# Kernel tuning notes

Measured on AMD Instinct MI355X. Metric: run time of the kernel, lower is better.

Reference implementation:

```python
import jax, jax.numpy as jnp
import numpy as np

N_HEAD = 16
D_HEAD = 64
D_MODEL = 1024
LN_EPS = 1e-5


def layer_norm(x, gamma, beta):
    mu = jnp.mean(x, axis=-1, keepdims=True)
    var = jnp.mean((x - mu) ** 2, axis=-1, keepdims=True)
    return (x - mu) * jax.lax.rsqrt(var + LN_EPS) * gamma + beta


def setup_inputs() -> dict:
    key = jax.random.key(0)
    ks = jax.random.split(key, 6)
    B, T = 2, 2048
    inp = jax.random.normal(ks[0], (B, T, D_MODEL), dtype=jnp.float32)
    # qkv_net: Linear(d_model, 3*n_head*d_head)
    W_qkv = jax.random.normal(ks[1], (3 * N_HEAD * D_HEAD, D_MODEL), dtype=jnp.float32) * (D_MODEL ** -0.5)
    b_qkv = jax.random.normal(ks[2], (3 * N_HEAD * D_HEAD,), dtype=jnp.float32) * 0.02
    # o_net: Linear(n_head*d_head, d_model, bias=False)
    W_o = jax.random.normal(ks[3], (D_MODEL, N_HEAD * D_HEAD), dtype=jnp.float32) * ((N_HEAD * D_HEAD) ** -0.5)
    gamma = jnp.ones((D_MODEL,), dtype=jnp.float32)
    beta = jnp.zeros((D_MODEL,), dtype=jnp.float32)
    return {"inp": inp, "W_qkv": W_qkv, "b_qkv": b_qkv, "W_o": W_o, "gamma": gamma, "beta": beta}


def reference(inp, W_qkv, b_qkv, W_o, gamma, beta):
    B, T, D = inp.shape
    H, dh = N_HEAD, D_HEAD
    scale = 1.0 / (dh ** 0.5)

    qkv = inp @ W_qkv.T + b_qkv                      # (B, T, 3*H*dh)
    head_q, head_k, head_v = jnp.split(qkv, 3, axis=2)
    # (B, T, H, dh) -> (B, H, T, dh)
    q = head_q.reshape(B, T, H, dh).transpose(0, 2, 1, 3)
    k = head_k.reshape(B, T, H, dh).transpose(0, 2, 1, 3)
    v = head_v.reshape(B, T, H, dh).transpose(0, 2, 1, 3)

    attn_score = jnp.einsum('bhqd,bhkd->bhqk', q, k) * scale  # (B, H, T, T)
    attn_prob = jax.nn.softmax(attn_score, axis=-1)           # dropatt is identity in eval
    attn_vec = jnp.einsum('bhqk,bhkd->bhqd', attn_prob, v)    # (B, H, T, dh)

    # Faithful to original: (B*H, T, dh) batch-major buffer is VIEWED as (H, B, T, dh)
    attn_vec = attn_vec.reshape(H, B, T, dh)
    attn_vec = attn_vec.transpose(1, 2, 0, 3).reshape(B, T, H * dh)

    attn_out = attn_vec @ W_o.T                                # dropout identity in eval
    return layer_norm(inp + attn_out, gamma, beta)
```

## Files before the change

### kernel.cpp

```cpp
#include <hip/hip_runtime.h>
#include <hip/hip_bf16.h>
#include <stdint.h>

typedef __bf16 bf16_t;
typedef __bf16 bf16x8 __attribute__((ext_vector_type(8)));
typedef __bf16 bf16x4 __attribute__((ext_vector_type(4)));
typedef float floatx4 __attribute__((ext_vector_type(4)));

#define QSCALE 0.180336879f

__device__ static inline void gll16(const void* g, void* l) {
    __builtin_amdgcn_global_load_lds((const __attribute__((address_space(1))) void*)g,
                                     (__attribute__((address_space(3))) void*)l, 16, 0, 0);
}

__global__ __launch_bounds__(256) void cvt_f32_bf16(const float* __restrict__ in,
                                                    bf16_t* __restrict__ out, int n4) {
    int i = blockIdx.x * 256 + threadIdx.x;
    if (i < n4) {
        float4 v = ((const float4*)in)[i];
        bf16x4 o;
        o[0] = (bf16_t)v.x; o[1] = (bf16_t)v.y; o[2] = (bf16_t)v.z; o[3] = (bf16_t)v.w;
        ((bf16x4*)out)[i] = o;
    }
}

__global__ __launch_bounds__(256, 3)
void gemm_qkv(const bf16_t* __restrict__ A, const bf16_t* __restrict__ Bw,
              const float* __restrict__ bias,
              bf16_t* __restrict__ qk, bf16_t* __restrict__ vT) {
    constexpr int K = 1024;
    __shared__ bf16_t lA[128 * 32];
    __shared__ bf16_t lB[128 * 32];
    const int tid  = threadIdx.x;
    const int lane = tid & 63, wave = tid >> 6;
    const int quad = lane >> 4, l16 = lane & 15;
    const int wy = wave >> 1, wx = wave & 1;
    const int bm = blockIdx.y * 128, bn = blockIdx.x * 128;

    const int c0 = tid, c1 = tid + 256;
    const bf16_t* Ap0 = A + (size_t)(bm + (c0 >> 2)) * K + (c0 & 3) * 8;
    const bf16_t* Ap1 = A + (size_t)(bm + (c1 >> 2)) * K + (c1 & 3) * 8;
    const bf16_t* Bp0 = Bw + (size_t)(bn + (c0 >> 2)) * K + (c0 & 3) * 8;
    const bf16_t* Bp1 = Bw + (size_t)(bn + (c1 >> 2)) * K + (c1 & 3) * 8;
    bf16_t* dA0 = &lA[(wave * 64) * 8];
    bf16_t* dA1 = &lA[(256 + wave * 64) * 8];
    bf16_t* dB0 = &lB[(wave * 64) * 8];
    bf16_t* dB1 = &lB[(256 + wave * 64) * 8];

    floatx4 acc[4][4] = {};

    for (int kt = 0; kt < K; kt += 32) {
        __syncthreads();
        gll16(Ap0 + kt, dA0);
        gll16(Ap1 + kt, dA1);
        gll16(Bp0 + kt, dB0);
        gll16(Bp1 + kt, dB1);
        __syncthreads();
        bf16x8 af[4], bfr[4];
#pragma unroll
        for (int i = 0; i < 4; i++) {
            af[i]  = *(const bf16x8*)(lA + (wy * 64 + i * 16 + l16) * 32 + quad * 8);
            bfr[i] = *(const bf16x8*)(lB + (wx * 64 + i * 16 + l16) * 32 + quad * 8);
        }
#pragma unroll
        for (int i = 0; i < 4; i++)
#pragma unroll
            for (int j = 0; j < 4; j++)
                acc[i][j] = __builtin_amdgcn_mfma_f32_16x16x32_bf16(af[i], bfr[j], acc[i][j], 0, 0, 0);
    }

    const bool is_v = (bn >= 2048);
#pragma unroll
    for (int j = 0; j < 4; j++) {
        const int n = bn + wx * 64 + j * 16 + l16;
        const float bv = bias[n];
        const bool isq = (n < 1024);
#pragma unroll
        for (int i = 0; i < 4; i++) {
            const int mbase = bm + wy * 64 + i * 16 + quad * 4;
            if (!is_v) {
#pragma unroll
                for (int r = 0; r < 4; r++) {
                    float c = acc[i][j][r] + bv;
                    if (isq) c *= QSCALE;
                    qk[(size_t)(mbase + r) * 2048 + n] = (bf16_t)c;
                }
            } else {
                const int nn = n - 2048;
                const int b  = mbase >> 11;
                const int t  = mbase & 2047;
                const int vrow = b * 1024 + nn;
                bf16x4 pack;
#pragma unroll
                for (int r = 0; r < 4; r++) pack[r] = (bf16_t)(acc[i][j][r] + bv);
                *(bf16x4*)(vT + (size_t)vrow * 2048 + t) = pack;
            }
        }
    }
}

__global__ __launch_bounds__(256, 2)
void attn_kernel(const bf16_t* __restrict__ qk, const bf16_t* __restrict__ vT,
                 bf16_t* __restrict__ av) {
    __shared__ bf16_t Kbuf[2][64 * 72];
    __shared__ bf16_t Vbuf[2][64 * 72];
    __shared__ bf16_t Pbuf[4][2][16 * 72];
    const int tid  = threadIdx.x;
    const int lane = tid & 63, wave = tid >> 6;
    const int quad = lane >> 4, l16 = lane & 15;
    const int bid = blockIdx.x;
    const int s  = bid & 31;
    const int hl = (s & 7) * 4 + (s >> 3);
    const int qt = bid >> 5;
    const int b = hl >> 4, h = hl & 15;

    const bf16_t* Qbase = qk + (size_t)(b * 2048 + qt * 128 + wave * 32) * 2048 + h * 64;
    const bf16_t* Kbase = qk + (size_t)(b * 2048) * 2048 + 1024 + h * 64;
    const bf16_t* Vbase = vT + (size_t)(hl * 64) * 2048;

    const int sr = tid >> 3;
    const int sc = (tid & 7) * 8;
    const bf16_t* Kg = Kbase + (size_t)sr * 2048 + sc;
    const bf16_t* Vg = Vbase + (size_t)sr * 2048 + sc;

    bf16x8 qf[2][2];
#pragma unroll
    for (int rt = 0; rt < 2; rt++)
#pragma unroll
        for (int kc = 0; kc < 2; kc++)
            qf[rt][kc] = *(const bf16x8*)(Qbase + (size_t)(rt * 16 + l16) * 2048 + kc * 32 + quad * 8);

    floatx4 accO[2][4] = {};
    float lacc[2] = {0.f, 0.f};

    {
        bf16x8 k0 = *(const bf16x8*)(Kg);
        bf16x8 k1 = *(const bf16x8*)(Kg + (size_t)32 * 2048);
        bf16x8 v0 = *(const bf16x8*)(Vg);
        bf16x8 v1 = *(const bf16x8*)(Vg + (size_t)32 * 2048);
        *(bf16x8*)&Kbuf[0][sr * 72 + sc] = k0;
        *(bf16x8*)&Kbuf[0][(sr + 32) * 72 + sc] = k1;
        *(bf16x8*)&Vbuf[0][sr * 72 + sc] = v0;
        *(bf16x8*)&Vbuf[0][(sr + 32) * 72 + sc] = v1;
    }

    for (int it = 0; it < 32; ++it) {
        const int cur = it & 1;
        __syncthreads();
        bf16x8 gk0, gk1, gv0, gv1;
        if (it < 31) {
            const bf16_t* kg = Kg + (size_t)(it + 1) * 64 * 2048;
            const bf16_t* vg = Vg + (it + 1) * 64;
            gk0 = *(const bf16x8*)(kg);
            gk1 = *(const bf16x8*)(kg + (size_t)32 * 2048);
            gv0 = *(const bf16x8*)(vg);
            gv1 = *(const bf16x8*)(vg + (size_t)32 * 2048);
        }
        floatx4 st[2][4] = {};
#pragma unroll
        for (int nt = 0; nt < 4; nt++) {
            const bf16_t* kr = &Kbuf[cur][(nt * 16 + l16) * 72 + quad * 8];
            bf16x8 k0 = *(const bf16x8*)(kr);
            bf16x8 k1 = *(const bf16x8*)(kr + 32);
            st[0][nt] = __builtin_amdgcn_mfma_f32_16x16x32_bf16(k0, qf[0][0], st[0][nt], 0, 0, 0);
            st[0][nt] = __builtin_amdgcn_mfma_f32_16x16x32_bf16(k1, qf[0][1], st[0][nt], 0, 0, 0);
            st[1][nt] = __builtin_amdgcn_mfma_f32_16x16x32_bf16(k0, qf[1][0], st[1][nt], 0, 0, 0);
            st[1][nt] = __builtin_amdgcn_mfma_f32_16x16x32_bf16(k1, qf[1][1], st[1][nt], 0, 0, 0);
        }
#pragma unroll
        for (int rt = 0; rt < 2; rt++) {
            float ls = 0.f;
#pragma unroll
            for (int nt = 0; nt < 4; nt++) {
                bf16x4 pk;
#pragma unroll
                for (int r = 0; r < 4; r++) {
                    float p = exp2f(st[rt][nt][r]);
                    ls += p;
                    pk[r] = (bf16_t)p;
                }
                *(bf16x4*)&Pbuf[wave][rt][l16 * 72 + nt * 16 + quad * 4] = pk;
            }
            lacc[rt] += ls;
        }
#pragma unroll
        for (int kc2 = 0; kc2 < 2; kc2++) {
            bf16x8 pf0 = *(const bf16x8*)&Pbuf[wave][0][l16 * 72 + kc2 * 32 + quad * 8];
            bf16x8 pf1 = *(const bf16x8*)&Pbuf[wave][1][l16 * 72 + kc2 * 32 + quad * 8];
#pragma unroll
            for (int ct = 0; ct < 4; ct++) {
                bf16x8 vf = *(const bf16x8*)&Vbuf[cur][(ct * 16 + l16) * 72 + kc2 * 32 + quad * 8];
                accO[0][ct] = __builtin_amdgcn_mfma_f32_16x16x32_bf16(pf0, vf, accO[0][ct], 0, 0, 0);
                accO[1][ct] = __builtin_amdgcn_mfma_f32_16x16x32_bf16(pf1, vf, accO[1][ct], 0, 0, 0);
            }
        }
        if (it < 31) {
            const int nxt = cur ^ 1;
            *(bf16x8*)&Kbuf[nxt][sr * 72 + sc] = gk0;
            *(bf16x8*)&Kbuf[nxt][(sr + 32) * 72 + sc] = gk1;
            *(bf16x8*)&Vbuf[nxt][sr * 72 + sc] = gv0;
            *(bf16x8*)&Vbuf[nxt][(sr + 32) * 72 + sc] = gv1;
        }
    }

    float linv[2];
#pragma unroll
    for (int rt = 0; rt < 2; rt++) {
        float l = lacc[rt];
        l += __shfl_xor(l, 16);
        l += __shfl_xor(l, 32);
        linv[rt] = 1.0f / l;
    }
    const int b2 = hl & 1;
    const int colb = (hl >> 1) * 64;
    bf16_t* outb = av + (size_t)(b2 * 2048 + qt * 128 + wave * 32) * 1024 + colb;
#pragma unroll
    for (int rt = 0; rt < 2; rt++) {
        float invq[4];
#pragma unroll
        for (int r = 0; r < 4; r++) invq[r] = __shfl(linv[rt], quad * 4 + r);
#pragma unroll
        for (int ct = 0; ct < 4; ct++)
#pragma unroll
            for (int r = 0; r < 4; r++)
                outb[(size_t)(rt * 16 + quad * 4 + r) * 1024 + ct * 16 + l16] =
                    (bf16_t)(accO[rt][ct][r] * invq[r]);
    }
}

__global__ __launch_bounds__(256, 3)
void gemm_o(const bf16_t* __restrict__ A, const bf16_t* __restrict__ Bw,
            float* __restrict__ out) {
    constexpr int K = 1024;
    __shared__ bf16_t lA[128 * 32];
    __shared__ bf16_t lB[128 * 32];
    const int tid  = threadIdx.x;
    const int lane = tid & 63, wave = tid >> 6;
    const int quad = lane >> 4, l16 = lane & 15;
    const int wy = wave >> 1, wx = wave & 1;
    const int bm = blockIdx.y * 128, bn = blockIdx.x * 128;

    const int c0 = tid, c1 = tid + 256;
    const bf16_t* Ap0 = A + (size_t)(bm + (c0 >> 2)) * K + (c0 & 3) * 8;
    const bf16_t* Ap1 = A + (size_t)(bm + (c1 >> 2)) * K + (c1 & 3) * 8;
    const bf16_t* Bp0 = Bw + (size_t)(bn + (c0 >> 2)) * K + (c0 & 3) * 8;
    const bf16_t* Bp1 = Bw + (size_t)(bn + (c1 >> 2)) * K + (c1 & 3) * 8;
    bf16_t* dA0 = &lA[(wave * 64) * 8];
    bf16_t* dA1 = &lA[(256 + wave * 64) * 8];
    bf16_t* dB0 = &lB[(wave * 64) * 8];
    bf16_t* dB1 = &lB[(256 + wave * 64) * 8];

    floatx4 acc[4][4] = {};
    for (int kt = 0; kt < K; kt += 32) {
        __syncthreads();
        gll16(Ap0 + kt, dA0);
        gll16(Ap1 + kt, dA1);
        gll16(Bp0 + kt, dB0);
        gll16(Bp1 + kt, dB1);
        __syncthreads();
        bf16x8 af[4], bfr[4];
#pragma unroll
        for (int i = 0; i < 4; i++) {
            af[i]  = *(const bf16x8*)(lA + (wy * 64 + i * 16 + l16) * 32 + quad * 8);
            bfr[i] = *(const bf16x8*)(lB + (wx * 64 + i * 16 + l16) * 32 + quad * 8);
        }
#pragma unroll
        for (int i = 0; i < 4; i++)
#pragma unroll
            for (int j = 0; j < 4; j++)
                acc[i][j] = __builtin_amdgcn_mfma_f32_16x16x32_bf16(af[i], bfr[j], acc[i][j], 0, 0, 0);
    }
#pragma unroll
    for (int j = 0; j < 4; j++) {
        const int n = bn + wx * 64 + j * 16 + l16;
#pragma unroll
        for (int i = 0; i < 4; i++) {
            const int mbase = bm + wy * 64 + i * 16 + quad * 4;
#pragma unroll
            for (int r = 0; r < 4; r++)
                out[(size_t)(mbase + r) * 1024 + n] = acc[i][j][r];
        }
    }
}

__global__ __launch_bounds__(256)
void ln_kernel(const float* __restrict__ inp, const float* __restrict__ ao,
               const float* __restrict__ gamma, const float* __restrict__ beta,
               float* __restrict__ out) {
    const int row = blockIdx.x, tid = threadIdx.x;
    const int wave = tid >> 6, lane = tid & 63;
    float4 a = ((const float4*)(inp + (size_t)row * 1024))[tid];
    float4 c = ((const float4*)(ao + (size_t)row * 1024))[tid];
    float x0 = a.x + c.x, x1 = a.y + c.y, x2 = a.z + c.z, x3 = a.w + c.w;
    float s = x0 + x1 + x2 + x3;
    float sq = x0 * x0 + x1 * x1 + x2 * x2 + x3 * x3;
#pragma unroll
    for (int mm = 32; mm >= 1; mm >>= 1) {
        s += __shfl_xor(s, mm);
        sq += __shfl_xor(sq, mm);
    }
    __shared__ float rs[4], rq[4];
    if (lane == 0) { rs[wave] = s; rq[wave] = sq; }
    __syncthreads();
    s = rs[0] + rs[1] + rs[2] + rs[3];
    sq = rq[0] + rq[1] + rq[2] + rq[3];
    const float mu = s * (1.0f / 1024.0f);
    const float var = sq * (1.0f / 1024.0f) - mu * mu;
    const float rstd = rsqrtf(var + 1e-5f);
    float4 g = ((const float4*)gamma)[tid], bt = ((const float4*)beta)[tid];
    float4 o;
    o.x = (x0 - mu) * rstd * g.x + bt.x;
    o.y = (x1 - mu) * rstd * g.y + bt.y;
    o.z = (x2 - mu) * rstd * g.z + bt.z;
    o.w = (x3 - mu) * rstd * g.w + bt.w;
    ((float4*)(out + (size_t)row * 1024))[tid] = o;
}

extern "C" void kernel_launch(void* const* d_in, const int* in_sizes, int n_in,
                              void* d_out, int out_size, void* d_ws, size_t ws_size,
                              hipStream_t stream) {
    const float* inp   = (const float*)d_in[0];
    const float* Wqkv  = (const float*)d_in[1];
    const float* bqkv  = (const float*)d_in[2];
    const float* Wo    = (const float*)d_in[3];
    const float* gamma = (const float*)d_in[4];
    const float* beta  = (const float*)d_in[5];
    float* out = (float*)d_out;

    char* ws = (char*)d_ws;
    bf16_t* inp_bf  = (bf16_t*)(ws);
    bf16_t* wqkv_bf = (bf16_t*)(ws + (8u << 20));
    bf16_t* wo_bf   = (bf16_t*)(ws + (14u << 20));
    bf16_t* qk_buf  = (bf16_t*)(ws + (16u << 20));
    bf16_t* vT_buf  = (bf16_t*)(ws + (32u << 20));
    bf16_t* av_buf  = (bf16_t*)(ws + (40u << 20));
    float*  ao_buf  = (float*)(ws + (48u << 20));

    cvt_f32_bf16<<<4096, 256, 0, stream>>>(inp, inp_bf, 4096 * 1024 / 4);
    cvt_f32_bf16<<<3072, 256, 0, stream>>>(Wqkv, wqkv_bf, 3072 * 1024 / 4);
    cvt_f32_bf16<<<1024, 256, 0, stream>>>(Wo, wo_bf, 1024 * 1024 / 4);

    gemm_qkv<<<dim3(24, 32), 256, 0, stream>>>(inp_bf, wqkv_bf, bqkv, qk_buf, vT_buf);
    attn_kernel<<<512, 256, 0, stream>>>(qk_buf, vT_buf, av_buf);
    gemm_o<<<dim3(8, 32), 256, 0, stream>>>(av_buf, wo_bf, ao_buf);
    ln_kernel<<<4096, 256, 0, stream>>>(inp, ao_buf, gamma, beta, out);
}
```

Baseline: 222.4 us.

## Fuse conversions, split attention LDS layout, shrink gemm_o tiles, raise occupancy

Three f32-to-bf16 conversion launches are merged into one kernel that picks its source by block index, saving launch overhead. The attention kernel moves from padded 72-wide LDS rows to two unpadded 32-wide halves, raises launch bounds to 3 blocks per CU, and uses the hardware exp2 builtin. It also processes the P·V product one row tile at a time. gemm_o switches to 64x128 tiles with twice as many blocks and 4 blocks per CU to fill the machine better. The attention change leaves a dead loop and computes exp2 twice per score, and the unpadded LDS rows may cause bank conflicts.

Result: faster. 210.4 us (-5.4%).

```diff
diff --git a/kernel.cpp b/kernel.cpp
--- a/kernel.cpp
+++ b/kernel.cpp
@@ -14,15 +14,23 @@
                                      (__attribute__((address_space(3))) void*)l, 16, 0, 0);
 }
 
-__global__ __launch_bounds__(256) void cvt_f32_bf16(const float* __restrict__ in,
-                                                    bf16_t* __restrict__ out, int n4) {
-    int i = blockIdx.x * 256 + threadIdx.x;
-    if (i < n4) {
-        float4 v = ((const float4*)in)[i];
-        bf16x4 o;
-        o[0] = (bf16_t)v.x; o[1] = (bf16_t)v.y; o[2] = (bf16_t)v.z; o[3] = (bf16_t)v.w;
-        ((bf16x4*)out)[i] = o;
-    }
+__global__ __launch_bounds__(256) void cvt_all(const float* __restrict__ inp,
+                                               const float* __restrict__ wqkv,
+                                               const float* __restrict__ wo,
+                                               bf16_t* __restrict__ o_inp,
+                                               bf16_t* __restrict__ o_wqkv,
+                                               bf16_t* __restrict__ o_wo) {
+    int blk = blockIdx.x;
+    const float* src;
+    bf16_t* dst;
+    if (blk < 4096)      { src = inp;  dst = o_inp; }
+    else if (blk < 7168) { src = wqkv; dst = o_wqkv; blk -= 4096; }
+    else                 { src = wo;   dst = o_wo;   blk -= 7168; }
+    int i = blk * 256 + threadIdx.x;
+    float4 v = ((const float4*)src)[i];
+    bf16x4 o;
+    o[0] = (bf16_t)v.x; o[1] = (bf16_t)v.y; o[2] = (bf16_t)v.z; o[3] = (bf16_t)v.w;
+    ((bf16x4*)dst)[i] = o;
 }
 
 __global__ __launch_bounds__(256, 3)
@@ -100,12 +108,12 @@
     }
 }
 
-__global__ __launch_bounds__(256, 2)
+__global__ __launch_bounds__(256, 3)
 void attn_kernel(const bf16_t* __restrict__ qk, const bf16_t* __restrict__ vT,
                  bf16_t* __restrict__ av) {
-    __shared__ bf16_t Kbuf[2][64 * 72];
-    __shared__ bf16_t Vbuf[2][64 * 72];
-    __shared__ bf16_t Pbuf[4][2][16 * 72];
+    __shared__ bf16_t Kbuf[2][2][64 * 32];
+    __shared__ bf16_t Vbuf[2][2][64 * 32];
+    __shared__ bf16_t Pbuf[4][2][16 * 32];
     const int tid  = threadIdx.x;
     const int lane = tid & 63, wave = tid >> 6;
     const int quad = lane >> 4, l16 = lane & 15;
@@ -120,9 +128,10 @@
     const bf16_t* Vbase = vT + (size_t)(hl * 64) * 2048;
 
     const int sr = tid >> 3;
-    const int sc = (tid & 7) * 8;
-    const bf16_t* Kg = Kbase + (size_t)sr * 2048 + sc;
-    const bf16_t* Vg = Vbase + (size_t)sr * 2048 + sc;
+    const int c8 = tid & 7;
+    const int half = c8 >> 2, ce = (c8 & 3) * 8;
+    const bf16_t* Kg = Kbase + (size_t)sr * 2048 + c8 * 8;
+    const bf16_t* Vg = Vbase + (size_t)sr * 2048 + c8 * 8;
 
     bf16x8 qf[2][2];
 #pragma unroll
@@ -139,10 +148,10 @@
         bf16x8 k1 = *(const bf16x8*)(Kg + (size_t)32 * 2048);
         bf16x8 v0 = *(const bf16x8*)(Vg);
         bf16x8 v1 = *(const bf16x8*)(Vg + (size_t)32 * 2048);
-        *(bf16x8*)&Kbuf[0][sr * 72 + sc] = k0;
-        *(bf16x8*)&Kbuf[0][(sr + 32) * 72 + sc] = k1;
-        *(bf16x8*)&Vbuf[0][sr * 72 + sc] = v0;
-        *(bf16x8*)&Vbuf[0][(sr + 32) * 72 + sc] = v1;
+        *(bf16x8*)&Kbuf[0][half][sr * 32 + ce] = k0;
+        *(bf16x8*)&Kbuf[0][half][(sr + 32) * 32 + ce] = k1;
+        *(bf16x8*)&Vbuf[0][half][sr * 32 + ce] = v0;
+        *(bf16x8*)&Vbuf[0][half][(sr + 32) * 32 + ce] = v1;
     }
 
     for (int it = 0; it < 32; ++it) {
@@ -160,9 +169,8 @@
         floatx4 st[2][4] = {};
 #pragma unroll
         for (int nt = 0; nt < 4; nt++) {
-            const bf16_t* kr = &Kbuf[cur][(nt * 16 + l16) * 72 + quad * 8];
-            bf16x8 k0 = *(const bf16x8*)(kr);
-            bf16x8 k1 = *(const bf16x8*)(kr + 32);
+            bf16x8 k0 = *(const bf16x8*)&Kbuf[cur][0][(nt * 16 + l16) * 32 + quad * 8];
+            bf16x8 k1 = *(const bf16x8*)&Kbuf[cur][1][(nt * 16 + l16) * 32 + quad * 8];
             st[0][nt] = __builtin_amdgcn_mfma_f32_16x16x32_bf16(k0, qf[0][0], st[0][nt], 0, 0, 0);
             st[0][nt] = __builtin_amdgcn_mfma_f32_16x16x32_bf16(k1, qf[0][1], st[0][nt], 0, 0, 0);
             st[1][nt] = __builtin_amdgcn_mfma_f32_16x16x32_bf16(k0, qf[1][0], st[1][nt], 0, 0, 0);
@@ -176,31 +184,48 @@
                 bf16x4 pk;
 #pragma unroll
                 for (int r = 0; r < 4; r++) {
-                    float p = exp2f(st[rt][nt][r]);
+                    float p = __builtin_amdgcn_exp2f(st[rt][nt][r]);
                     ls += p;
                     pk[r] = (bf16_t)p;
                 }
-                *(bf16x4*)&Pbuf[wave][rt][l16 * 72 + nt * 16 + quad * 4] = pk;
+                *(bf16x4*)&Pbuf[wave][nt >> 1][l16 * 32 + (nt & 1) * 16 + quad * 4] = pk;
             }
             lacc[rt] += ls;
         }
 #pragma unroll
         for (int kc2 = 0; kc2 < 2; kc2++) {
-            bf16x8 pf0 = *(const bf16x8*)&Pbuf[wave][0][l16 * 72 + kc2 * 32 + quad * 8];
-            bf16x8 pf1 = *(const bf16x8*)&Pbuf[wave][1][l16 * 72 + kc2 * 32 + quad * 8];
-#pragma unroll
-            for (int ct = 0; ct < 4; ct++) {
-                bf16x8 vf = *(const bf16x8*)&Vbuf[cur][(ct * 16 + l16) * 72 + kc2 * 32 + quad * 8];
-                accO[0][ct] = __builtin_amdgcn_mfma_f32_16x16x32_bf16(pf0, vf, accO[0][ct], 0, 0, 0);
-                accO[1][ct] = __builtin_amdgcn_mfma_f32_16x16x32_bf16(pf1, vf, accO[1][ct], 0, 0, 0);
+            bf16x8 pf0 = *(const bf16x8*)&Pbuf[wave][kc2][l16 * 32 + quad * 8];
+            pf0 = pf0;
+            break;
+        }
+        {
+#pragma unroll
+            for (int rt = 0; rt < 2; rt++) {
+#pragma unroll
+                for (int nt = 0; nt < 4; nt++) {
+                    bf16x4 pk;
+#pragma unroll
+                    for (int r = 0; r < 4; r++)
+                        pk[r] = (bf16_t)__builtin_amdgcn_exp2f(st[rt][nt][r]);
+                    *(bf16x4*)&Pbuf[wave][nt >> 1][l16 * 32 + (nt & 1) * 16 + quad * 4] = pk;
+                }
+#pragma unroll
+                for (int kc2 = 0; kc2 < 2; kc2++) {
+                    bf16x8 pf = *(const bf16x8*)&Pbuf[wave][kc2][l16 * 32 + quad * 8];
+#pragma unroll
+                    for (int ct = 0; ct < 4; ct++) {
+                        bf16x8 vf = *(const bf16x8*)&Vbuf[cur][kc2][(ct * 16 + l16) * 32 + quad * 8];
+                        accO[rt][ct] = __builtin_amdgcn_mfma_f32_16x16x32_bf16(pf, vf, accO[rt][ct], 0, 0, 0);
+                    }
+                }
             }
         }
         if (it < 31) {
             const int nxt = cur ^ 1;
-            *(bf16x8*)&Kbuf[nxt][sr * 72 + sc] = gk0;
-            *(bf16x8*)&Kbuf[nxt][(sr + 32) * 72 + sc] = gk1;
-            *(bf16x8*)&Vbuf[nxt][sr * 72 + sc] = gv0;
-            *(bf16x8*)&Vbuf[nxt][(sr + 32) * 72 + sc] = gv1;
+            *(bf16x8*)&Kbuf[nxt][half][sr * 32 + ce] = gk0;
+            *(bf16x8*)&Kbuf[nxt][half][(sr + 32) * 32 + ce] = gk1;
+            *(bf16x8*)&Vbuf[nxt][half][sr * 32 + ce] = gv0;
+            *(bf16x8*)&Vbuf[nxt][half][(sr + 32) * 32 + ce] = gv1;
         }
     }
 
@@ -229,44 +254,43 @@
     }
 }
 
-__global__ __launch_bounds__(256, 3)
+__global__ __launch_bounds__(256, 4)
 void gemm_o(const bf16_t* __restrict__ A, const bf16_t* __restrict__ Bw,
             float* __restrict__ out) {
     constexpr int K = 1024;
-    __shared__ bf16_t lA[128 * 32];
+    __shared__ bf16_t lA[64 * 32];
     __shared__ bf16_t lB[128 * 32];
     const int tid  = threadIdx.x;
     const int lane = tid & 63, wave = tid >> 6;
     const int quad = lane >> 4, l16 = lane & 15;
     const int wy = wave >> 1, wx = wave & 1;
-    const int bm = blockIdx.y * 128, bn = blockIdx.x * 128;
-
-    const int c0 = tid, c1 = tid + 256;
-    const bf16_t* Ap0 = A + (size_t)(bm + (c0 >> 2)) * K + (c0 & 3) * 8;
-    const bf16_t* Ap1 = A + (size_t)(bm + (c1 >> 2)) * K + (c1 & 3) * 8;
-    const bf16_t* Bp0 = Bw + (size_t)(bn + (c0 >> 2)) * K + (c0 & 3) * 8;
-    const bf16_t* Bp1 = Bw + (size_t)(bn + (c1 >> 2)) * K + (c1 & 3) * 8;
-    bf16_t* dA0 = &lA[(wave * 64) * 8];
-    bf16_t* dA1 = &lA[(256 + wave * 64) * 8];
+    const int bm = blockIdx.y * 64, bn = blockIdx.x * 128;
+
+    const int ca = tid;
+    const int cb0 = tid, cb1 = tid + 256;
+    const bf16_t* Ap  = A + (size_t)(bm + (ca >> 2)) * K + (ca & 3) * 8;
+    const bf16_t* Bp0 = Bw + (size_t)(bn + (cb0 >> 2)) * K + (cb0 & 3) * 8;
+    const bf16_t* Bp1 = Bw + (size_t)(bn + (cb1 >> 2)) * K + (cb1 & 3) * 8;
+    bf16_t* dA  = &lA[(wave * 64) * 8];
     bf16_t* dB0 = &lB[(wave * 64) * 8];
     bf16_t* dB1 = &lB[(256 + wave * 64) * 8];
 
-    floatx4 acc[4][4] = {};
+    floatx4 acc[2][4] = {};
     for (int kt = 0; kt < K; kt += 32) {
         __syncthreads();
-        gll16(Ap0 + kt, dA0);
-        gll16(Ap1 + kt, dA1);
+        gll16(Ap + kt, dA);
         gll16(Bp0 + kt, dB0);
         gll16(Bp1 + kt, dB1);
         __syncthreads();
-        bf16x8 af[4], bfr[4];
-#pragma unroll
-        for (int i = 0; i < 4; i++) {
-            af[i]  = *(const bf16x8*)(lA + (wy * 64 + i * 16 + l16) * 32 + quad * 8);
-            bfr[i] = *(const bf16x8*)(lB + (wx * 64 + i * 16 + l16) * 32 + quad * 8);
-        }
-#pragma unroll
-        for (int i = 0; i < 4; i++)
+        bf16x8 af[2], bfr[4];
+#pragma unroll
+        for (int i = 0; i < 2; i++)
+            af[i] = *(const bf16x8*)(lA + (wy * 32 + i * 16 + l16) * 32 + quad * 8);
+#pragma unroll
+        for (int j = 0; j < 4; j++)
+            bfr[j] = *(const bf16x8*)(lB + (wx * 64 + j * 16 + l16) * 32 + quad * 8);
+#pragma unroll
+        for (int i = 0; i < 2; i++)
 #pragma unroll
             for (int j = 0; j < 4; j++)
                 acc[i][j] = __builtin_amdgcn_mfma_f32_16x16x32_bf16(af[i], bfr[j], acc[i][j], 0, 0, 0);
@@ -275,8 +299,8 @@
     for (int j = 0; j < 4; j++) {
         const int n = bn + wx * 64 + j * 16 + l16;
 #pragma unroll
-        for (int i = 0; i < 4; i++) {
-            const int mbase = bm + wy * 64 + i * 16 + quad * 4;
+        for (int i = 0; i < 2; i++) {
+            const int mbase = bm + wy * 32 + i * 16 + quad * 4;
 #pragma unroll
             for (int r = 0; r < 4; r++)
                 out[(size_t)(mbase + r) * 1024 + n] = acc[i][j][r];
@@ -337,12 +361,9 @@
     bf16_t* av_buf  = (bf16_t*)(ws + (40u << 20));
     float*  ao_buf  = (float*)(ws + (48u << 20));
 
-    cvt_f32_bf16<<<4096, 256, 0, stream>>>(inp, inp_bf, 4096 * 1024 / 4);
-    cvt_f32_bf16<<<3072, 256, 0, stream>>>(Wqkv, wqkv_bf, 3072 * 1024 / 4);
-    cvt_f32_bf16<<<1024, 256, 0, stream>>>(Wo, wo_bf, 1024 * 1024 / 4);
-
+    cvt_all<<<8192, 256, 0, stream>>>(inp, Wqkv, Wo, inp_bf, wqkv_bf, wo_bf);
     gemm_qkv<<<dim3(24, 32), 256, 0, stream>>>(inp_bf, wqkv_bf, bqkv, qk_buf, vT_buf);
     attn_kernel<<<512, 256, 0, stream>>>(qk_buf, vT_buf, av_buf);
-    gemm_o<<<dim3(8, 32), 256, 0, stream>>>(av_buf, wo_bf, ao_buf);
+    gemm_o<<<dim3(8, 64), 256, 0, stream>>>(av_buf, wo_bf, ao_buf);
     ln_kernel<<<4096, 256, 0, stream>>>(inp, ao_buf, gamma, beta, out);
 }
```
